# Kernel optimization log

Measured on AMD Instinct MI355X. Metric: run time of the kernel, lower is better.

Reference implementation:

```python
import jax, jax.numpy as jnp
import numpy as np

H, HKV, D, W = 64, 8, 64, 128          # heads, kv heads, head_dim, sliding window
G = H // HKV                            # query heads per kv head
HID = 2880
THETA = 150000.0
SCALE = D ** -0.5
NEG = -1e30


def _rope(x, positions):
    # x: [B,S,h,D]; GPT-NeoX style rotate_half RoPE
    half = D // 2
    inv_freq = 1.0 / (THETA ** (jnp.arange(0, half, dtype=jnp.float32) / half))
    ang = positions.astype(jnp.float32)[:, None] * inv_freq          # [S, D/2]
    cos = jnp.cos(ang)[None, :, None, :]
    sin = jnp.sin(ang)[None, :, None, :]
    x1, x2 = x[..., :half], x[..., half:]
    return jnp.concatenate([x1 * cos - x2 * sin, x2 * cos + x1 * sin], axis=-1)


def setup_inputs() -> dict:
    key = jax.random.key(0)
    ks = jax.random.split(key, 6)
    B, S = 1, 2048
    return {
        "hidden_states": jax.random.normal(ks[0], (B, S, HID), jnp.float32),
        "positions": jnp.arange(S, dtype=jnp.int32),
        "w_qkv": jax.random.normal(ks[1], (HID, (H + 2 * HKV) * D), jnp.float32) * 0.02,
        "b_qkv": jax.random.normal(ks[2], ((H + 2 * HKV) * D,), jnp.float32) * 0.02,
        "w_o": jax.random.normal(ks[3], (H * D, HID), jnp.float32) * 0.02,
        "b_o": jax.random.normal(ks[4], (HID,), jnp.float32) * 0.02,
        "sinks": jax.random.normal(ks[5], (H,), jnp.float32),
    }


def reference(hidden_states, positions, w_qkv, b_qkv, w_o, b_o, sinks):
    B, S, _ = hidden_states.shape
    qkv = hidden_states @ w_qkv + b_qkv                               # [B,S,(H+2Hkv)*D]
    q, k, v = jnp.split(qkv, [H * D, H * D + HKV * D], axis=-1)
    Q = q.reshape(B, S, H, D)
    K = k.reshape(B, S, HKV, D)
    V = v.reshape(B, S, HKV, D)
    Q = _rope(Q, positions)
    K = _rope(K, positions)

    # banded (sliding-window) key/value gather: query i sees keys i-W+1..i
    offsets = jnp.arange(W) - (W - 1)                                 # [-(W-1)..0]
    kidx = jnp.arange(S)[:, None] + offsets                           # [S,W]
    valid = kidx >= 0
    kidx = jnp.maximum(kidx, 0)
    Kw = K[:, kidx]                                                    # [B,S,W,HKV,D]
    Vw = V[:, kidx]

    Qr = Q.reshape(B, S, HKV, G, D)                                    # GQA grouping
    scores = jnp.einsum('bskgd,bswkd->bskgw', Qr, Kw) * SCALE          # [B,S,HKV,G,W]
    scores = jnp.where(valid[None, :, None, None, :], scores, NEG)

    sink = sinks.reshape(HKV, G)[None, None]                           # [1,1,HKV,G]
    m = jnp.maximum(scores.max(axis=-1), sink)                         # [B,S,HKV,G]
    p = jnp.exp(scores - m[..., None])
    denom = p.sum(axis=-1) + jnp.exp(sink - m)                         # sink in normalizer
    out = jnp.einsum('bskgw,bswkd->bskgd', p, Vw) / denom[..., None]

    out = out.reshape(B, S, H * D)
    return out @ w_o + b_o
```

## Files before the change

### kernel.cpp

```cpp
#include <hip/hip_runtime.h>

typedef unsigned short u16;
typedef __bf16 bf16x8 __attribute__((ext_vector_type(8)));
typedef float f32x4 __attribute__((ext_vector_type(4)));
typedef unsigned short u16x8 __attribute__((ext_vector_type(8)));

#define QKV_N 5120
#define SEQ 2048
#define ATTN_K 4096
#define K1 2880
#define SCALE 0.125f
#define NEGINF -1e30f

__device__ __forceinline__ u16 f2bf(float f) {
  unsigned int u = __builtin_bit_cast(unsigned int, f);
  u = (u + 0x7FFFu + ((u >> 16) & 1u)) >> 16;
  return (u16)u;
}
__device__ __forceinline__ float bf2f(u16 u) {
  unsigned int x = ((unsigned int)u) << 16;
  return __builtin_bit_cast(float, x);
}

#define MFMA16(a, b, c) __builtin_amdgcn_mfma_f32_16x16x32_bf16((a), (b), (c), 0, 0, 0)

__device__ __forceinline__ void gl_lds16(const u16* g, u16* l) {
  __builtin_amdgcn_global_load_lds(
      (const __attribute__((address_space(1))) unsigned int*)(const void*)g,
      (__attribute__((address_space(3))) unsigned int*)(void*)l, 16, 0, 0);
}

__device__ __forceinline__ bf16x8 fragrd(const u16* base, int row, int rb) {
  return *(const bf16x8*)((const char*)(base + row * 32) + rb);
}

__device__ __forceinline__ bf16x8 lds_frag(const u16* mat, int row, int kh, int lg) {
  int off = row * 128 + ((kh * 64 + lg * 16) ^ ((row & 7) << 4));
  return *(const bf16x8*)((const char*)mat + off);
}

__global__ __launch_bounds__(256) void k_prep(const int* __restrict__ pos,
                                              float2* __restrict__ tab,
                                              const float* __restrict__ hs,
                                              u16* __restrict__ hsb,
                                              const float* __restrict__ wqkv,
                                              u16* __restrict__ wqkvT,
                                              const float* __restrict__ wo,
                                              u16* __restrict__ woT) {
  __shared__ float tile[32][33];
  const int blk = blockIdx.x;
  if (blk < 256) {
    int t = blk * 256 + threadIdx.x;
    int s = t >> 5, i = t & 31;
    float freq = powf(150000.0f, -(float)i * (1.0f / 32.0f));
    float ang = (float)pos[s] * freq;
    float sv, cv;
    sincosf(ang, &sv, &cv);
    tab[t] = make_float2(cv, sv);
  } else if (blk < 6016) {
    int i = (blk - 256) * 256 + threadIdx.x;
    float4 v = *(const float4*)(hs + (size_t)i * 4);
    ushort4 o;
    o.x = f2bf(v.x); o.y = f2bf(v.y); o.z = f2bf(v.z); o.w = f2bf(v.w);
    ((ushort4*)hsb)[i] = o;
  } else {
    const float* in;
    u16* out;
    int Kin, Kout, Nd, Npad, bx, by;
    if (blk < 20416) {
      int q = blk - 6016;
      bx = q % 160; by = q / 160;
      in = wqkv; out = wqkvT; Kin = 2880; Kout = K1; Nd = 5120; Npad = 5120;
    } else {
      int q = blk - 20416;
      bx = q % 92; by = q / 92;
      in = wo; out = woT; Kin = 4096; Kout = 4096; Nd = 2880; Npad = 2944;
    }
    int n0 = bx * 32, k0 = by * 32;
    int c = threadIdx.x & 31, r0 = threadIdx.x >> 5;
#pragma unroll
    for (int j = 0; j < 4; j++) {
      int r = r0 + j * 8;
      float v = 0.f;
      if (n0 + c < Nd && k0 + r < Kin) v = in[(size_t)(k0 + r) * Nd + n0 + c];
      tile[r][c] = v;
    }
    __syncthreads();
#pragma unroll
    for (int j = 0; j < 4; j++) {
      int rr = r0 + j * 8;
      int n = n0 + rr;
      if (n < Npad) out[(size_t)n * Kout + k0 + c] = f2bf(tile[c][rr]);
    }
  }
}

__global__ __launch_bounds__(256, 2) void k_gemm1(const u16* __restrict__ Ag,
                                                  const u16* __restrict__ Bg,
                                                  const float* __restrict__ bias,
                                                  u16* __restrict__ C) {
  __shared__ u16 lds_[2][18432];
  u16* L = &lds_[0][0];
  const int tid = threadIdx.x;
  const int lane = tid & 63, wave = tid >> 6;
  const int wm = wave >> 1, wn = wave & 1;
  const int lr = lane & 15, lg = lane >> 4;
  const int bid = blockIdx.x;
  const int xcd = bid & 7, j = bid >> 3;
  const int m0 = (j >> 2) * 128;
  const int n0 = (xcd * 4 + (j & 3)) * 160;

  f32x4 acc[4][5] = {};
  bf16x8 Bf[5], Af0, Af1;

  const int rb = (lg * 16) ^ (((lr >> 1) & 3) << 4);
  const int arow = tid >> 2;
  const int axs = ((tid & 3) ^ ((tid >> 3) & 3)) << 3;

  size_t boff[5];
#pragma unroll
  for (int r_ = 0; r_ < 5; r_++) {
    int e = r_ * 2048 + tid * 8;
    int bkh = (e >= 5120) ? 1 : 0;
    int re = e - bkh * 5120;
    int brow = re >> 5;
    int bch = (re >> 3) & 3;
    int bps = bch ^ ((brow >> 1) & 3);
    boff[r_] = (size_t)(n0 + brow) * K1 + bkh * 32 + bps * 8;
  }

#define STA(b, kh, kt, r_)                                                      \
  gl_lds16(Ag + (size_t)(m0 + (r_) * 64 + arow) * K1 + (kt) + (kh) * 32 + axs,  \
           L + (b) * 18432 + (kh) * 4096 + (r_) * 2048 + wave * 512)
#define STB(b, kt, r_)                                                          \
  gl_lds16(Bg + boff[r_] + (kt), L + (b) * 18432 + 8192 + (r_) * 2048 + wave * 512)
#define RDB(b, kh)                                                              \
  { _Pragma("unroll") for (int nf = 0; nf < 5; nf++)                            \
      Bf[nf] = fragrd(L + (b) * 18432 + 8192 + (kh) * 5120,                     \
                      wn * 80 + nf * 16 + lr, rb); }
#define RDA(b, kh, mf0_)                                                        \
  { Af0 = fragrd(L + (b) * 18432 + (kh) * 4096, wm * 64 + (mf0_) * 16 + lr, rb); \
    Af1 = fragrd(L + (b) * 18432 + (kh) * 4096, wm * 64 + ((mf0_) + 1) * 16 + lr, rb); }
#define MM(ma, mb)                                                              \
  { __builtin_amdgcn_s_setprio(1);                                              \
    _Pragma("unroll") for (int nf = 0; nf < 5; nf++) {                          \
      acc[ma][nf] = MFMA16(Af0, Bf[nf], acc[ma][nf]);                           \
      acc[mb][nf] = MFMA16(Af1, Bf[nf], acc[mb][nf]); }                         \
    __builtin_amdgcn_s_setprio(0); }
#define BAR __builtin_amdgcn_s_barrier();
#define VM4 asm volatile("s_waitcnt vmcnt(4)" ::: "memory");
#define VM0 asm volatile("s_waitcnt vmcnt(0)" ::: "memory");

  STA(0, 0, 0, 0); STA(0, 0, 0, 1);
  STB(0, 0, 0); STB(0, 0, 1); STB(0, 0, 2); STB(0, 0, 3); STB(0, 0, 4);
  STA(0, 1, 0, 0); STA(0, 1, 0, 1);
  VM4 BAR

  for (int t = 0; t < 45; t++) {
    const int b = t & 1, nb = b ^ 1;
    const int kt1 = (t + 1) * 64;
    const bool st = (t < 44);
    RDB(b, 0) RDA(b, 0, 0)
    if (st) { STA(nb, 0, kt1, 0); STA(nb, 0, kt1, 1); STB(nb, kt1, 0); }
    BAR MM(0, 1) BAR
    RDA(b, 0, 2)
    if (st) { STB(nb, kt1, 1); STB(nb, kt1, 2); VM4 } else { VM0 }
    BAR MM(2, 3) BAR
    RDB(b, 1) RDA(b, 1, 0)
    if (st) { STB(nb, kt1, 3); STB(nb, kt1, 4); }
    BAR MM(0, 1) BAR
    RDA(b, 1, 2)
    if (st) { STA(nb, 1, kt1, 0); STA(nb, 1, kt1, 1); VM4 }
    BAR MM(2, 3) BAR
  }
#undef STA
#undef STB
#undef RDB
#undef RDA
#undef MM
#undef VM4
#undef VM0

#pragma unroll
  for (int mf = 0; mf < 4; mf++)
#pragma unroll
    for (int nf = 0; nf < 5; nf++) {
      int col = n0 + wn * 80 + nf * 16 + lr;
      float bv = bias[col];
#pragma unroll
      for (int rg = 0; rg < 4; rg++) {
        int row = m0 + wm * 64 + mf * 16 + lg * 4 + rg;
        C[(size_t)row * QKV_N + col] = f2bf(acc[mf][nf][rg] + bv);
      }
    }
}

__global__ __launch_bounds__(256, 2) void k_gemm2(const u16* __restrict__ Ag,
                                                  const u16* __restrict__ Bg,
                                                  const float* __restrict__ bias,
                                                  float* __restrict__ C) {
  __shared__ u16 ldsbuf[2][14336];
  const int tid = threadIdx.x;
  const int lane = tid & 63, wave = tid >> 6;
  const int wm = wave >> 1, wn = wave & 1;
  const int lr = lane & 15, lg = lane >> 4;
  int bid = blockIdx.x;
  int l = (bid & 7) * 60 + (bid >> 3);
  const int m0 = (l & 15) * 128, n0 = (l >> 4) * 96;

  f32x4 acc[4][3] = {};

  const int srow = wave * 8 + (lane >> 3);
  const int sc = ((lane & 7) ^ (lane >> 3)) << 3;
  const u16* gA = Ag + (size_t)(m0 + srow) * ATTN_K + sc;
  const u16* gB = Bg + (size_t)(n0 + srow) * ATTN_K + sc;

#define G2_STAGE(kt, b)                                                          \
  {                                                                              \
    u16* Ab = &ldsbuf[b][0];                                                     \
    u16* Bb = &ldsbuf[b][8192];                                                  \
    _Pragma("unroll") for (int r = 0; r < 4; r++)                                \
      gl_lds16(gA + (size_t)(r * 32) * ATTN_K + (kt), Ab + (r * 32 + wave * 8) * 64); \
    _Pragma("unroll") for (int r = 0; r < 3; r++)                                \
      gl_lds16(gB + (size_t)(r * 32) * ATTN_K + (kt), Bb + (r * 32 + wave * 8) * 64); \
  }

  G2_STAGE(0, 0)
  G2_STAGE(64, 1)
  asm volatile("s_waitcnt vmcnt(7)" ::: "memory");
  __builtin_amdgcn_s_barrier();

  for (int t = 0; t < 64; t++) {
    const int b = t & 1;
    const u16* La = &ldsbuf[b][0];
    const u16* Lb = &ldsbuf[b][8192];
    bf16x8 Bf[3][2];
#pragma unroll
    for (int nf = 0; nf < 3; nf++)
#pragma unroll
      for (int kh = 0; kh < 2; kh++)
        Bf[nf][kh] = lds_frag(Lb, wn * 48 + nf * 16 + lr, kh, lg);
    bf16x8 Af[2][2];
#pragma unroll
    for (int mi = 0; mi < 2; mi++)
#pragma unroll
      for (int kh = 0; kh < 2; kh++)
        Af[mi][kh] = lds_frag(La, wm * 64 + mi * 16 + lr, kh, lg);
#pragma unroll
    for (int q = 0; q < 2; q++) {
      bf16x8 An[2][2];
      if (q < 1) {
#pragma unroll
        for (int mi = 0; mi < 2; mi++)
#pragma unroll
          for (int kh = 0; kh < 2; kh++)
            An[mi][kh] = lds_frag(La, wm * 64 + ((q + 1) * 2 + mi) * 16 + lr, kh, lg);
      }
      __builtin_amdgcn_s_setprio(1);
#pragma unroll
      for (int mi = 0; mi < 2; mi++)
#pragma unroll
        for (int nf = 0; nf < 3; nf++)
#pragma unroll
          for (int kh = 0; kh < 2; kh++)
            acc[q * 2 + mi][nf] = MFMA16(Af[mi][kh], Bf[nf][kh], acc[q * 2 + mi][nf]);
      __builtin_amdgcn_s_setprio(0);
      if (q < 1) {
#pragma unroll
        for (int mi = 0; mi < 2; mi++)
#pragma unroll
          for (int kh = 0; kh < 2; kh++)
            Af[mi][kh] = An[mi][kh];
      }
    }
    __builtin_amdgcn_s_barrier();
    if (t <= 61) {
      G2_STAGE((t + 2) * 64, b)
      asm volatile("s_waitcnt vmcnt(7)" ::: "memory");
    } else {
      asm volatile("s_waitcnt vmcnt(0)" ::: "memory");
    }
    __builtin_amdgcn_s_barrier();
  }
#undef G2_STAGE

#pragma unroll
  for (int mi = 0; mi < 4; mi++)
#pragma unroll
    for (int ni = 0; ni < 3; ni++) {
      int row = m0 + wm * 64 + mi * 16 + lg * 4;
      int col = n0 + wn * 48 + ni * 16 + lr;
      float bv = bias[col];
#pragma unroll
      for (int rg = 0; rg < 4; rg++)
        C[(size_t)(row + rg) * 2880 + col] = acc[mi][ni][rg] + bv;
    }
}

__global__ __launch_bounds__(512, 2) void k_attn(const u16* __restrict__ qkv,
                                                 const float* __restrict__ sinks,
                                                 const float2* __restrict__ tab,
                                                 u16* __restrict__ out) {
  __shared__ u16 Klds[192 * 64];
  __shared__ u16 Vt[64 * 200];
  __shared__ u16 Pslab[8 * 32 * 40];
  const int hk = blockIdx.y;
  const int s0 = blockIdx.x * 64;
  const int kb = s0 - 127;
  const int tid = threadIdx.x;
  const int lane = tid & 63, w = tid >> 6;
  const int lr = lane & 15, lg = lane >> 4;
  const int head = hk * 8 + w;

  for (int u = tid; u < 192 * 4; u += 512) {
    int key = u >> 2, c = u & 3;
    int kidx = kb + key;
    u16x8 v1 = {0, 0, 0, 0, 0, 0, 0, 0}, v2 = v1;
    if (kidx >= 0 && kidx < SEQ) {
      const u16* base = qkv + (size_t)kidx * QKV_N + 4096 + hk * 64;
      u16x8 x1 = *(const u16x8*)(base + c * 8);
      u16x8 x2 = *(const u16x8*)(base + 32 + c * 8);
      const float2* cs = tab + (size_t)kidx * 32 + c * 8;
#pragma unroll
      for (int jj = 0; jj < 8; jj++) {
        float f1 = bf2f(x1[jj]), f2 = bf2f(x2[jj]);
        float2 t = cs[jj];
        v1[jj] = f2bf(f1 * t.x - f2 * t.y);
        v2[jj] = f2bf(f2 * t.x + f1 * t.y);
      }
    }
    int o1 = (key * 128 + c * 16) ^ ((key & 7) << 4);
    int o2 = (key * 128 + (c + 4) * 16) ^ ((key & 7) << 4);
    *(u16x8*)((char*)Klds + o1) = v1;
    *(u16x8*)((char*)Klds + o2) = v2;
  }
  for (int e4 = tid; e4 < 192 * 16; e4 += 512) {
    int key = e4 >> 4, d0 = (e4 & 15) * 4;
    int kidx = kb + key;
    ushort4 v = {0, 0, 0, 0};
    if (kidx >= 0 && kidx < SEQ)
      v = *(const ushort4*)(qkv + (size_t)kidx * QKV_N + 4608 + hk * 64 + d0);
    Vt[(d0 + 0) * 200 + key] = v.x;
    Vt[(d0 + 1) * 200 + key] = v.y;
    Vt[(d0 + 2) * 200 + key] = v.z;
    Vt[(d0 + 3) * 200 + key] = v.w;
  }
  __syncthreads();

  const float sink = sinks[head];
  u16* slab = &Pslab[w * 32 * 40];
  f32x4 zz = {0.f, 0.f, 0.f, 0.f};

  for (int qs = 0; qs < 2; qs++) {
    const int qbase = s0 + qs * 32;
    const int koff = qs * 32;

    bf16x8 qf[2][2];
#pragma unroll
    for (int rt = 0; rt < 2; rt++) {
      int s = qbase + rt * 16 + lr;
      const u16* base = qkv + (size_t)s * QKV_N + head * 64 + lg * 8;
      u16x8 r0 = *(const u16x8*)(base);
      u16x8 r1 = *(const u16x8*)(base + 32);
      const float2* cs = tab + (size_t)s * 32 + lg * 8;
      u16x8 y0, y1;
#pragma unroll
      for (int jj = 0; jj < 8; jj++) {
        float f1 = bf2f(r0[jj]), f2 = bf2f(r1[jj]);
        float2 t = cs[jj];
        y0[jj] = f2bf(f1 * t.x - f2 * t.y);
        y1[jj] = f2bf(f2 * t.x + f1 * t.y);
      }
      qf[rt][0] = __builtin_bit_cast(bf16x8, y0);
      qf[rt][1] = __builtin_bit_cast(bf16x8, y1);
    }

    f32x4 sc[2][10];
#pragma unroll
    for (int rt = 0; rt < 2; rt++)
#pragma unroll
      for (int nt = 0; nt < 10; nt++) sc[rt][nt] = zz;
#pragma unroll
    for (int nt = 0; nt < 10; nt++) {
      int key = koff + nt * 16 + lr;
#pragma unroll
      for (int ks = 0; ks < 2; ks++) {
        int off = (key * 128 + ks * 64 + lg * 16) ^ ((key & 7) << 4);
        bf16x8 kf = *(const bf16x8*)((const char*)Klds + off);
        sc[0][nt] = MFMA16(qf[0][ks], kf, sc[0][nt]);
        sc[1][nt] = MFMA16(qf[1][ks], kf, sc[1][nt]);
      }
    }

#pragma unroll
    for (int rt = 0; rt < 2; rt++)
#pragma unroll
      for (int nt = 0; nt < 10; nt++)
#pragma unroll
        for (int rg = 0; rg < 4; rg++) {
          int qq = rt * 16 + lg * 4 + rg;
          int jl = nt * 16 + lr;
          bool valid = (jl >= qq) && (jl <= qq + 127) && ((kb + koff + jl) >= 0);
          sc[rt][nt][rg] = valid ? sc[rt][nt][rg] * SCALE : NEGINF;
        }

    float den[2][4];
#pragma unroll
    for (int rt = 0; rt < 2; rt++)
#pragma unroll
      for (int rg = 0; rg < 4; rg++) {
        float m = NEGINF;
#pragma unroll
        for (int nt = 0; nt < 10; nt++) m = fmaxf(m, sc[rt][nt][rg]);
#pragma unroll
        for (int x = 1; x < 16; x <<= 1) m = fmaxf(m, __shfl_xor(m, x, 64));
        m = fmaxf(m, sink);
        float sum = 0.f;
#pragma unroll
        for (int nt = 0; nt < 10; nt++) {
          float p = __expf(sc[rt][nt][rg] - m);
          sc[rt][nt][rg] = p;
          sum += p;
        }
#pragma unroll
        for (int x = 1; x < 16; x <<= 1) sum += __shfl_xor(sum, x, 64);
        den[rt][rg] = sum + __expf(sink - m);
      }

    f32x4 oacc[2][4];
#pragma unroll
    for (int rt = 0; rt < 2; rt++)
#pragma unroll
      for (int dn = 0; dn < 4; dn++) oacc[rt][dn] = zz;
#pragma unroll
    for (int kt = 0; kt < 5; kt++) {
#pragma unroll
      for (int rt = 0; rt < 2; rt++)
#pragma unroll
        for (int j2 = 0; j2 < 2; j2++)
#pragma unroll
          for (int rg = 0; rg < 4; rg++)
            slab[(rt * 16 + lg * 4 + rg) * 40 + j2 * 16 + lr] =
                f2bf(sc[rt][kt * 2 + j2][rg]);
      asm volatile("s_waitcnt lgkmcnt(0)" ::: "memory");
      __builtin_amdgcn_sched_barrier(0);
      bf16x8 pf0 = *(const bf16x8*)&slab[lr * 40 + lg * 8];
      bf16x8 pf1 = *(const bf16x8*)&slab[(16 + lr) * 40 + lg * 8];
#pragma unroll
      for (int dn = 0; dn < 4; dn++) {
        bf16x8 vf = *(const bf16x8*)&Vt[(dn * 16 + lr) * 200 + koff + kt * 32 + lg * 8];
        oacc[0][dn] = MFMA16(pf0, vf, oacc[0][dn]);
        oacc[1][dn] = MFMA16(pf1, vf, oacc[1][dn]);
      }
    }

#pragma unroll
    for (int rt = 0; rt < 2; rt++)
#pragma unroll
      for (int dn = 0; dn < 4; dn++)
#pragma unroll
        for (int rg = 0; rg < 4; rg++) {
          int s = qbase + rt * 16 + lg * 4 + rg;
          float val = oacc[rt][dn][rg] / den[rt][rg];
          out[(size_t)s * ATTN_K + head * 64 + dn * 16 + lr] = f2bf(val);
        }
  }
}

extern "C" void kernel_launch(void* const* d_in, const int* in_sizes, int n_in,
                              void* d_out, int out_size, void* d_ws, size_t ws_size,
                              hipStream_t stream) {
  const float* hs = (const float*)d_in[0];
  const int* pos = (const int*)d_in[1];
  const float* wqkv = (const float*)d_in[2];
  const float* bqkv = (const float*)d_in[3];
  const float* wo = (const float*)d_in[4];
  const float* bo = (const float*)d_in[5];
  const float* sinks = (const float*)d_in[6];
  float* out = (float*)d_out;

  char* ws = (char*)d_ws;
  u16* qkvb = (u16*)(ws + 0);
  u16* hsb = (u16*)(ws + 41943040);
  u16* wqkvT = (u16*)(ws + 53739520);
  u16* attnb = (u16*)(ws + 41943040);
  u16* woT = (u16*)(ws + 83230720);
  float2* tab = (float2*)(ws + 107347968);

  k_prep<<<32192, 256, 0, stream>>>(pos, tab, hs, hsb, wqkv, wqkvT, wo, woT);
  k_gemm1<<<512, 256, 0, stream>>>(hsb, wqkvT, bqkv, qkvb);
  k_attn<<<dim3(32, 8), 512, 0, stream>>>(qkvb, sinks, tab, attnb);
  k_gemm2<<<480, 256, 0, stream>>>(attnb, woT, bo, out);
}
```

Baseline: 180.0 us.

## Load GEMM1 A fragments directly from global into registers, skip LDS staging

The QKV projection GEMM no longer stages the A (activation) tile through LDS. Each wave now loads its A fragments straight from global memory into registers with double-buffered X/Y register sets, and only B goes through LDS. This shrinks LDS use and cuts LDS write/read traffic for A, and the wait counts are retuned to fit. The cost is that A rows are now read from global separately by each wave column (wn), so global/L2 traffic for A doubles. The per-lane loads are also less coalesced, which could expose latency.

```diff
diff --git a/kernel.cpp b/kernel.cpp
--- a/kernel.cpp
+++ b/kernel.cpp
@@ -99,7 +99,7 @@
                                                   const u16* __restrict__ Bg,
                                                   const float* __restrict__ bias,
                                                   u16* __restrict__ C) {
-  __shared__ u16 lds_[2][18432];
+  __shared__ u16 lds_[2][10240];
   u16* L = &lds_[0][0];
   const int tid = threadIdx.x;
   const int lane = tid & 63, wave = tid >> 6;
@@ -111,11 +111,11 @@
   const int n0 = (xcd * 4 + (j & 3)) * 160;
 
   f32x4 acc[4][5] = {};
-  bf16x8 Bf[5], Af0, Af1;
+  bf16x8 Bf[5], X0, X1, Y0, Y1;
 
   const int rb = (lg * 16) ^ (((lr >> 1) & 3) << 4);
-  const int arow = tid >> 2;
-  const int axs = ((tid & 3) ^ ((tid >> 3) & 3)) << 3;
+
+  const u16* aA = Ag + (size_t)(m0 + wm * 64 + lr) * K1 + lg * 8;
 
   size_t boff[5];
 #pragma unroll
@@ -129,56 +129,58 @@
     boff[r_] = (size_t)(n0 + brow) * K1 + bkh * 32 + bps * 8;
   }
 
-#define STA(b, kh, kt, r_)                                                      \
-  gl_lds16(Ag + (size_t)(m0 + (r_) * 64 + arow) * K1 + (kt) + (kh) * 32 + axs,  \
-           L + (b) * 18432 + (kh) * 4096 + (r_) * 2048 + wave * 512)
 #define STB(b, kt, r_)                                                          \
-  gl_lds16(Bg + boff[r_] + (kt), L + (b) * 18432 + 8192 + (r_) * 2048 + wave * 512)
+  gl_lds16(Bg + boff[r_] + (kt), L + (b) * 10240 + (r_) * 2048 + wave * 512)
 #define RDB(b, kh)                                                              \
   { _Pragma("unroll") for (int nf = 0; nf < 5; nf++)                            \
-      Bf[nf] = fragrd(L + (b) * 18432 + 8192 + (kh) * 5120,                     \
+      Bf[nf] = fragrd(L + (b) * 10240 + (kh) * 5120,                            \
                       wn * 80 + nf * 16 + lr, rb); }
-#define RDA(b, kh, mf0_)                                                        \
-  { Af0 = fragrd(L + (b) * 18432 + (kh) * 4096, wm * 64 + (mf0_) * 16 + lr, rb); \
-    Af1 = fragrd(L + (b) * 18432 + (kh) * 4096, wm * 64 + ((mf0_) + 1) * 16 + lr, rb); }
-#define MM(ma, mb)                                                              \
+#define LDA(d0, d1, mf0_, kk)                                                   \
+  { d0 = *(const bf16x8*)(aA + (size_t)(mf0_) * 16 * K1 + (kk));                \
+    d1 = *(const bf16x8*)(aA + (size_t)((mf0_) + 1) * 16 * K1 + (kk)); }
+#define MM(Aa, Ab, ma, mb)                                                      \
   { __builtin_amdgcn_s_setprio(1);                                              \
     _Pragma("unroll") for (int nf = 0; nf < 5; nf++) {                          \
-      acc[ma][nf] = MFMA16(Af0, Bf[nf], acc[ma][nf]);                           \
-      acc[mb][nf] = MFMA16(Af1, Bf[nf], acc[mb][nf]); }                         \
+      acc[ma][nf] = MFMA16(Aa, Bf[nf], acc[ma][nf]);                            \
+      acc[mb][nf] = MFMA16(Ab, Bf[nf], acc[mb][nf]); }                          \
     __builtin_amdgcn_s_setprio(0); }
 #define BAR __builtin_amdgcn_s_barrier();
+#define VM6 asm volatile("s_waitcnt vmcnt(6)" ::: "memory");
+#define VM5 asm volatile("s_waitcnt vmcnt(5)" ::: "memory");
 #define VM4 asm volatile("s_waitcnt vmcnt(4)" ::: "memory");
+#define VM2 asm volatile("s_waitcnt vmcnt(2)" ::: "memory");
 #define VM0 asm volatile("s_waitcnt vmcnt(0)" ::: "memory");
 
-  STA(0, 0, 0, 0); STA(0, 0, 0, 1);
   STB(0, 0, 0); STB(0, 0, 1); STB(0, 0, 2); STB(0, 0, 3); STB(0, 0, 4);
-  STA(0, 1, 0, 0); STA(0, 1, 0, 1);
-  VM4 BAR
+  LDA(X0, X1, 0, 0)
+  VM2 BAR
 
   for (int t = 0; t < 45; t++) {
     const int b = t & 1, nb = b ^ 1;
-    const int kt1 = (t + 1) * 64;
+    const int kt = t * 64, kt1 = kt + 64;
     const bool st = (t < 44);
-    RDB(b, 0) RDA(b, 0, 0)
-    if (st) { STA(nb, 0, kt1, 0); STA(nb, 0, kt1, 1); STB(nb, kt1, 0); }
-    BAR MM(0, 1) BAR
-    RDA(b, 0, 2)
-    if (st) { STB(nb, kt1, 1); STB(nb, kt1, 2); VM4 } else { VM0 }
-    BAR MM(2, 3) BAR
-    RDB(b, 1) RDA(b, 1, 0)
-    if (st) { STB(nb, kt1, 3); STB(nb, kt1, 4); }
-    BAR MM(0, 1) BAR
-    RDA(b, 1, 2)
-    if (st) { STA(nb, 1, kt1, 0); STA(nb, 1, kt1, 1); VM4 }
-    BAR MM(2, 3) BAR
-  }
-#undef STA
+    RDB(b, 0)
+    LDA(Y0, Y1, 2, kt)
+    if (st) { STB(nb, kt1, 0); STB(nb, kt1, 1); VM4 } else { VM2 }
+    BAR MM(X0, X1, 0, 1) BAR
+    LDA(X0, X1, 0, kt + 32)
+    if (st) { STB(nb, kt1, 2); STB(nb, kt1, 3); VM6 } else { VM2 }
+    BAR MM(Y0, Y1, 2, 3) BAR
+    RDB(b, 1)
+    LDA(Y0, Y1, 2, kt + 32)
+    if (st) { STB(nb, kt1, 4); VM5 } else { VM2 }
+    BAR MM(X0, X1, 0, 1) BAR
+    if (st) { LDA(X0, X1, 0, kt1) VM2 } else { VM0 }
+    BAR MM(Y0, Y1, 2, 3) BAR
+  }
 #undef STB
 #undef RDB
-#undef RDA
+#undef LDA
 #undef MM
+#undef VM6
+#undef VM5
 #undef VM4
+#undef VM2
 #undef VM0
 
 #pragma unroll
```

Measured after the change: 215.3 us. 19.7% more time.
